# Kernel tuning notes

Hardware: AMD Instinct MI355X
Metric: run time of the kernel (lower is better)

Reference implementation:

```python
import jax, jax.numpy as jnp
import numpy as np

D_MODEL = 1024
NUM_HEADS = 16
D_K = D_MODEL // NUM_HEADS


def setup_inputs() -> dict:
    key = jax.random.key(0)
    ks = jax.random.split(key, 8)
    B, S = 2, 2048
    query = jax.random.normal(ks[0], (B, S, D_MODEL), dtype=jnp.float32)
    k_in = jax.random.normal(ks[1], (B, S, D_MODEL), dtype=jnp.float32)
    value = jax.random.normal(ks[2], (B, S, D_MODEL), dtype=jnp.float32)
    # causal mask: True = masked out (upper triangle above diagonal)
    mask = jnp.triu(jnp.ones((S, S), dtype=bool), k=1)[None, None, :, :]
    scale = 1.0 / np.sqrt(D_MODEL)
    W_q = jax.random.normal(ks[3], (D_MODEL, D_MODEL), dtype=jnp.float32) * scale
    W_k = jax.random.normal(ks[4], (D_MODEL, D_MODEL), dtype=jnp.float32) * scale
    W_v = jax.random.normal(ks[5], (D_MODEL, D_MODEL), dtype=jnp.float32) * scale
    W_o = jax.random.normal(ks[6], (D_MODEL, D_MODEL), dtype=jnp.float32) * scale
    return {"query": query, "key": k_in, "value": value, "mask": mask,
            "W_q": W_q, "W_k": W_k, "W_v": W_v, "W_o": W_o}


def _split(x):
    # [B, S, d_model] -> [B, h, S, d_k]
    B, S, _ = x.shape
    return x.reshape(B, S, NUM_HEADS, D_K).transpose(0, 2, 1, 3)


def reference(query, key, value, mask, W_q, W_k, W_v, W_o):
    # torch nn.Linear(bias=False): y = x @ W.T
    Q = _split(query @ W_q.T)   # [B, h, Sq, d_k]
    K = _split(key @ W_k.T)     # [B, h, Sk, d_k]
    V = _split(value @ W_v.T)   # [B, h, Sk, d_k]
    scores = jnp.einsum('bhqd,bhkd->bhqk', Q, K) / jnp.sqrt(jnp.float32(D_K))
    scores = jnp.where(mask, -jnp.inf, scores)
    attn_w = jax.nn.softmax(scores, axis=-1)
    attn_w = jnp.nan_to_num(attn_w, nan=0.0)
    out = jnp.einsum('bhqk,bhkd->bhqd', attn_w, V)  # [B, h, Sq, d_k]
    B, _, Sq, _ = out.shape
    merged = out.transpose(0, 2, 1, 3).reshape(B, Sq, D_MODEL)
    return merged @ W_o.T
```

## Files before the change

### kernel.cpp

```cpp
#include <hip/hip_runtime.h>
#include <hip/hip_bf16.h>
#include <stdint.h>

typedef __attribute__((ext_vector_type(4))) float f32x4;
typedef __attribute__((ext_vector_type(8))) __bf16 bf16x8;
typedef __attribute__((ext_vector_type(4))) unsigned short us4;
typedef __attribute__((ext_vector_type(8))) unsigned short us8;

#define SEQ 2048
#define DMODEL 1024
#define NH 16
#define DK 64
#define MTOT 4096

__device__ __forceinline__ unsigned short f2bf(float x) {
  union { float f; unsigned int u; } v; v.f = x;
  unsigned int r = v.u + 0x7fffu + ((v.u >> 16) & 1u);
  return (unsigned short)(r >> 16);
}

__device__ __forceinline__ unsigned int cvtpk(float lo, float hi) {
  unsigned int r;
  asm("v_cvt_pk_bf16_f32 %0, %1, %2" : "=v"(r) : "v"(lo), "v"(hi));
  return r;
}

__device__ __forceinline__ f32x4 mfma_bf16(bf16x8 a, bf16x8 b, f32x4 c) {
  return __builtin_amdgcn_mfma_f32_16x16x32_bf16(a, b, c, 0, 0, 0);
}

__device__ __forceinline__ void gload16(const unsigned short* g, unsigned short* l) {
  __builtin_amdgcn_global_load_lds((__attribute__((address_space(1))) void*)g,
                                   (__attribute__((address_space(3))) void*)l,
                                   16, 0, 0);
}

__global__ void cvt_w(const float* __restrict__ s0, const float* __restrict__ s1,
                      const float* __restrict__ s2, const float* __restrict__ s3,
                      unsigned short* __restrict__ d0, unsigned short* __restrict__ d1,
                      unsigned short* __restrict__ d2, unsigned short* __restrict__ d3) {
  const int y = blockIdx.y;
  const float* s = y == 0 ? s0 : y == 1 ? s1 : y == 2 ? s2 : s3;
  unsigned short* d = y == 0 ? d0 : y == 1 ? d1 : y == 2 ? d2 : d3;
  const int n4 = DMODEL * DMODEL / 4;
  const int stride = gridDim.x * blockDim.x;
  for (int i = blockIdx.x * blockDim.x + threadIdx.x; i < n4; i += stride) {
    f32x4 v = reinterpret_cast<const f32x4*>(s)[i];
    us4 o;
    o.x = f2bf(v.x); o.y = f2bf(v.y); o.z = f2bf(v.z); o.w = f2bf(v.w);
    reinterpret_cast<us4*>(d)[i] = o;
  }
}

__global__ __launch_bounds__(256) void gemm_qkv(
    const float* __restrict__ xq, const float* __restrict__ xk, const float* __restrict__ xv,
    const unsigned short* __restrict__ bwq, const unsigned short* __restrict__ bwk,
    const unsigned short* __restrict__ bwv,
    unsigned short* __restrict__ Qh, unsigned short* __restrict__ Kh,
    unsigned short* __restrict__ Vt) {
  const int z = blockIdx.z;
  const float* A = z == 0 ? xq : (z == 1 ? xk : xv);
  const unsigned short* B = z == 0 ? bwq : (z == 1 ? bwk : bwv);
  const float scale = z == 0 ? 0.18033688011112042f : 1.0f;

  __shared__ __align__(16) unsigned short lA[128 * 32];
  __shared__ __align__(16) unsigned short lB[128 * 32];
  const int tid = threadIdx.x;
  const int lane = tid & 63;
  const int wid = tid >> 6;
  const int l15 = lane & 15, l4 = lane >> 4;
  const int bm = blockIdx.x, bn = blockIdx.y;
  const int wr = wid >> 1, wc = wid & 1;

  f32x4 acc[4][4] = {};

  const int chunk0 = (wid * 2 + 0) * 64 + lane;
  const int chunk1 = (wid * 2 + 1) * 64 + lane;
  const int ar0 = chunk0 >> 2, ac0 = chunk0 & 3;
  const int ar1 = chunk1 >> 2, ac1 = chunk1 & 3;
  const float* gAf0 = A + (size_t)(bm * 128 + ar0) * 1024 + ac0 * 8;
  const float* gAf1 = A + (size_t)(bm * 128 + ar1) * 1024 + ac1 * 8;
  const unsigned short* gB0 = B + (size_t)(bn * 128 + ar0) * 1024 + (ac0 ^ (ar0 & 3)) * 8;
  const unsigned short* gB1 = B + (size_t)(bn * 128 + ar1) * 1024 + (ac1 ^ (ar1 & 3)) * 8;
  unsigned short* wA0 = lA + ar0 * 32 + ((ac0 ^ (ar0 & 3)) * 8);
  unsigned short* wA1 = lA + ar1 * 32 + ((ac1 ^ (ar1 & 3)) * 8);
  unsigned short* lB0 = lB + (wid * 2 + 0) * 512;
  unsigned short* lB1 = lB + (wid * 2 + 1) * 512;

  f32x4 ra0 = *reinterpret_cast<const f32x4*>(gAf0);
  f32x4 ra1 = *reinterpret_cast<const f32x4*>(gAf0 + 4);
  f32x4 rb0 = *reinterpret_cast<const f32x4*>(gAf1);
  f32x4 rb1 = *reinterpret_cast<const f32x4*>(gAf1 + 4);

  const int sx = l15 & 3;

  for (int kt = 0; kt < 1024; kt += 32) {
    __syncthreads();
    union { us8 h; unsigned int u[4]; } p0, p1;
    p0.u[0] = cvtpk(ra0.x, ra0.y); p0.u[1] = cvtpk(ra0.z, ra0.w);
    p0.u[2] = cvtpk(ra1.x, ra1.y); p0.u[3] = cvtpk(ra1.z, ra1.w);
    p1.u[0] = cvtpk(rb0.x, rb0.y); p1.u[1] = cvtpk(rb0.z, rb0.w);
    p1.u[2] = cvtpk(rb1.x, rb1.y); p1.u[3] = cvtpk(rb1.z, rb1.w);
    *reinterpret_cast<us8*>(wA0) = p0.h;
    *reinterpret_cast<us8*>(wA1) = p1.h;
    gload16(gB0 + kt, lB0);
    gload16(gB1 + kt, lB1);
    __syncthreads();

    if (kt + 32 < 1024) {
      ra0 = *reinterpret_cast<const f32x4*>(gAf0 + kt + 32);
      ra1 = *reinterpret_cast<const f32x4*>(gAf0 + kt + 36);
      rb0 = *reinterpret_cast<const f32x4*>(gAf1 + kt + 32);
      rb1 = *reinterpret_cast<const f32x4*>(gAf1 + kt + 36);
    }

    bf16x8 af[4], bfr[4];
#pragma unroll
    for (int i = 0; i < 4; ++i)
      af[i] = *reinterpret_cast<const bf16x8*>(
          &lA[(wr * 64 + i * 16 + l15) * 32 + ((l4 ^ sx) * 8)]);
#pragma unroll
    for (int j = 0; j < 4; ++j)
      bfr[j] = *reinterpret_cast<const bf16x8*>(
          &lB[(wc * 64 + j * 16 + l15) * 32 + ((l4 ^ sx) * 8)]);
    if (z < 2) {
#pragma unroll
      for (int i = 0; i < 4; ++i)
#pragma unroll
        for (int j = 0; j < 4; ++j)
          acc[i][j] = mfma_bf16(bfr[j], af[i], acc[i][j]);
    } else {
#pragma unroll
      for (int i = 0; i < 4; ++i)
#pragma unroll
        for (int j = 0; j < 4; ++j)
          acc[i][j] = mfma_bf16(af[i], bfr[j], acc[i][j]);
    }
  }

  const int row0 = bm * 128 + wr * 64;
  const int col0 = bn * 128 + wc * 64;

  if (z < 2) {
    unsigned short* out = z ? Kh : Qh;
#pragma unroll
    for (int i = 0; i < 4; ++i) {
      const int m = row0 + i * 16 + l15;
      const int b = m >> 11, s = m & 2047;
#pragma unroll
      for (int j = 0; j < 4; ++j) {
        const int n0 = col0 + j * 16 + l4 * 4;
        const int h = n0 >> 6, dd = n0 & 63;
        union { us4 h4; unsigned int u[2]; } pk;
        pk.u[0] = cvtpk(acc[i][j][0] * scale, acc[i][j][1] * scale);
        pk.u[1] = cvtpk(acc[i][j][2] * scale, acc[i][j][3] * scale);
        *reinterpret_cast<us4*>(&out[(size_t)(b * NH + h) * (SEQ * DK) + s * DK + dd]) = pk.h4;
      }
    }
  } else {
#pragma unroll
    for (int i = 0; i < 4; ++i) {
      const int m0 = row0 + i * 16 + l4 * 4;
      const int b = m0 >> 11, s0 = m0 & 2047;
      const int g = (s0 >> 2) & 7;
      const int col = (s0 & ~31) + ((g & 3) << 3) + ((g >> 2) << 2);
#pragma unroll
      for (int j = 0; j < 4; ++j) {
        const int n = col0 + j * 16 + l15;
        const int h = n >> 6, dd = n & 63;
        union { us4 h4; unsigned int u[2]; } pk;
        pk.u[0] = cvtpk(acc[i][j][0], acc[i][j][1]);
        pk.u[1] = cvtpk(acc[i][j][2], acc[i][j][3]);
        *reinterpret_cast<us4*>(&Vt[(size_t)(b * NH + h) * (DK * SEQ) + dd * SEQ + col]) = pk.h4;
      }
    }
  }
}

__global__ __launch_bounds__(512) void gemm_o(const unsigned short* __restrict__ A,
                                              const unsigned short* __restrict__ B,
                                              float* __restrict__ out) {
  __shared__ __align__(16) unsigned short lA3[3][128 * 64];
  __shared__ __align__(16) unsigned short lB3[3][128 * 64];

  const int tid = threadIdx.x;
  const int lane = tid & 63, wid = tid >> 6;
  const int l15 = lane & 15, l4 = lane >> 4;
  const int bm = blockIdx.x, bn = blockIdx.y;
  const int wr = wid >> 1, wc = wid & 1;

  f32x4 acc[2][4] = {};

  const int r8 = lane >> 3, c8 = lane & 7;
  const unsigned short* gAs[2];
  const unsigned short* gBs[2];
  int dstoff[2];
#pragma unroll
  for (int is = 0; is < 2; ++is) {
    const int rbase = is * 64 + wid * 8;
    gAs[is] = A + (size_t)(bm * 128 + rbase + r8) * 1024 + (c8 ^ r8) * 8;
    gBs[is] = B + (size_t)(bn * 128 + rbase + r8) * 1024 + (c8 ^ r8) * 8;
    dstoff[is] = rbase * 64;
  }

#define STAGE_O(t, buf)                                         \
  {                                                             \
    const int kb = (t) * 64;                                    \
    gload16(gAs[0] + kb, &lA3[buf][dstoff[0]]);                 \
    gload16(gAs[1] + kb, &lA3[buf][dstoff[1]]);                 \
    gload16(gBs[0] + kb, &lB3[buf][dstoff[0]]);                 \
    gload16(gBs[1] + kb, &lB3[buf][dstoff[1]]);                 \
  }

  STAGE_O(0, 0);
  STAGE_O(1, 1);

#pragma unroll 1
  for (int t = 0; t < 16; ++t) {
    if (t + 1 < 16) {
      asm volatile("s_waitcnt vmcnt(4)" ::: "memory");
    } else {
      asm volatile("s_waitcnt vmcnt(0)" ::: "memory");
    }
    __builtin_amdgcn_sched_barrier(0);
    __builtin_amdgcn_s_barrier();
    __builtin_amdgcn_sched_barrier(0);

    if (t + 2 < 16) {
      const int pb = (t + 2) % 3;
      STAGE_O(t + 2, pb);
    }

    const unsigned short* La = lA3[t % 3];
    const unsigned short* Lb = lB3[t % 3];
#pragma unroll
    for (int kk = 0; kk < 2; ++kk) {
      bf16x8 af[2], bf[4];
#pragma unroll
      for (int i = 0; i < 2; ++i) {
        const int row = wr * 32 + i * 16 + l15;
        af[i] = *reinterpret_cast<const bf16x8*>(
            &La[row * 64 + (((kk * 4 + l4) ^ (l15 & 7)) * 8)]);
      }
#pragma unroll
      for (int j = 0; j < 4; ++j) {
        const int row = wc * 64 + j * 16 + l15;
        bf[j] = *reinterpret_cast<const bf16x8*>(
            &Lb[row * 64 + (((kk * 4 + l4) ^ (l15 & 7)) * 8)]);
      }
#pragma unroll
      for (int i = 0; i < 2; ++i)
#pragma unroll
        for (int j = 0; j < 4; ++j)
          acc[i][j] = mfma_bf16(bf[j], af[i], acc[i][j]);
    }
  }
#undef STAGE_O

  const int row0 = bm * 128 + wr * 32;
  const int col0 = bn * 128 + wc * 64;
#pragma unroll
  for (int i = 0; i < 2; ++i) {
    const int m = row0 + i * 16 + l15;
#pragma unroll
    for (int j = 0; j < 4; ++j) {
      const int n0 = col0 + j * 16 + l4 * 4;
      *reinterpret_cast<f32x4*>(&out[(size_t)m * DMODEL + n0]) = acc[i][j];
    }
  }
}

__global__ __launch_bounds__(512, 2) void attn_kernel(const unsigned short* __restrict__ Qh,
                                                      const unsigned short* __restrict__ Kh,
                                                      const unsigned short* __restrict__ Vt,
                                                      unsigned short* __restrict__ Mg) {
  __shared__ __align__(16) unsigned short Kl[4][64 * 64];
  __shared__ __align__(16) unsigned short Vl[4][64 * 64];

  const int tid = threadIdx.x;
  const int lane = tid & 63;
  const int w = tid >> 6;
  const int l15 = lane & 15, l4 = lane >> 4;

  const int d = blockIdx.x;
  const int xcd = d & 7;
  const int j = d >> 3;
  const int bh = (j >> 3) * 8 + xcd;
  const int x = j & 7;

  const unsigned short* Qb = Qh + (size_t)bh * SEQ * DK;
  const unsigned short* Kb = Kh + (size_t)bh * SEQ * DK;
  const unsigned short* Vb = Vt + (size_t)bh * DK * SEQ;
  const int bq = bh >> 4, hh = bh & 15;
  unsigned short* Mbase = Mg + (size_t)bq * SEQ * DMODEL + hh * DK;

  const int srow = lane >> 3;
  const int sswz = (lane & 7) ^ srow;
  const unsigned short* KsrcB = Kb + (size_t)(w * 8 + srow) * DK + sswz * 8;
  const unsigned short* VsrcB = Vb + (size_t)(w * 8 + srow) * SEQ + sswz * 8;

  const int l7 = l15 & 7;

  const int taus[2] = {15 - x, x};

#pragma unroll 1
  for (int seg = 0; seg < 2; ++seg) {
    const int tau = taus[seg];
    const int qbase = tau * 128;
    const int q0w = qbase + w * 16;
    const int nt = 2 * tau + 2;

    __syncthreads();

    bf16x8 qf0 = *reinterpret_cast<const bf16x8*>(Qb + (size_t)(q0w + l15) * DK + l4 * 8);
    bf16x8 qf1 = *reinterpret_cast<const bf16x8*>(Qb + (size_t)(q0w + l15) * DK + 32 + l4 * 8);

    f32x4 o[4] = {};
    float mrow = -__builtin_inff();
    float lrow = 0.0f;

    gload16(KsrcB, &Kl[0][w * 512]);
    gload16(VsrcB, &Vl[0][w * 512]);
    gload16(KsrcB + (size_t)64 * DK, &Kl[1][w * 512]);
    gload16(VsrcB + 64, &Vl[1][w * 512]);

    const int S = nt >> 1;
#pragma unroll 1
    for (int s = 0; s < S; ++s) {
      const int t0 = s << 1;
      const int kbase0 = t0 << 6;

      asm volatile("s_waitcnt vmcnt(0)" ::: "memory");
      __builtin_amdgcn_sched_barrier(0);
      __builtin_amdgcn_s_barrier();
      __builtin_amdgcn_sched_barrier(0);

      if (t0 + 2 < nt) {
        gload16(KsrcB + (size_t)(kbase0 + 128) * DK, &Kl[(t0 + 2) & 3][w * 512]);
        gload16(VsrcB + (kbase0 + 128), &Vl[(t0 + 2) & 3][w * 512]);
        gload16(KsrcB + (size_t)(kbase0 + 192) * DK, &Kl[(t0 + 3) & 3][w * 512]);
        gload16(VsrcB + (kbase0 + 192), &Vl[(t0 + 3) & 3][w * 512]);
      }

#pragma unroll
      for (int u = 0; u < 2; ++u) {
        const int t = t0 + u;
        const int kbase = t << 6;
        if (kbase >= q0w + 16) continue;
        const unsigned short* Kc = Kl[t & 3];
        const unsigned short* Vc = Vl[t & 3];

        f32x4 sc[4];
        __builtin_amdgcn_s_setprio(1);
#pragma unroll
        for (int c = 0; c < 4; ++c) {
          const int krow = c * 16 + l15;
          bf16x8 kf0 = *reinterpret_cast<const bf16x8*>(&Kc[krow * 64 + ((l4 ^ l7) * 8)]);
          bf16x8 kf1 = *reinterpret_cast<const bf16x8*>(&Kc[krow * 64 + (((4 + l4) ^ l7) * 8)]);
          f32x4 z = {0.f, 0.f, 0.f, 0.f};
          z = mfma_bf16(kf0, qf0, z);
          sc[c] = mfma_bf16(kf1, qf1, z);
        }
        __builtin_amdgcn_s_setprio(0);

        if (kbase + 63 > q0w) {
          const int qg = q0w + l15;
#pragma unroll
          for (int c = 0; c < 4; ++c) {
            const int kp = kbase + c * 16 + l4 * 4;
#pragma unroll
            for (int r = 0; r < 4; ++r)
              if (kp + r > qg) sc[c][r] = -__builtin_inff();
          }
        }

        f32x4 mv = sc[0];
#pragma unroll
        for (int c = 1; c < 4; ++c)
#pragma unroll
          for (int r = 0; r < 4; ++r) mv[r] = fmaxf(mv[r], sc[c][r]);
        float pm = fmaxf(fmaxf(mv[0], mv[1]), fmaxf(mv[2], mv[3]));
        if (!__all(pm - mrow <= 8.0f)) {
          pm = fmaxf(pm, __shfl_xor(pm, 16));
          pm = fmaxf(pm, __shfl_xor(pm, 32));
          const float mn = fmaxf(mrow, pm);
          const float al = __builtin_amdgcn_exp2f(mrow - mn);
          mrow = mn;
          lrow *= al;
#pragma unroll
          for (int dd = 0; dd < 4; ++dd)
#pragma unroll
            for (int r = 0; r < 4; ++r) o[dd][r] *= al;
        }
        union PB { bf16x8 v; unsigned int u[4]; } pbv[2];
        f32x4 sv = {0.f, 0.f, 0.f, 0.f};
#pragma unroll
        for (int c = 0; c < 4; ++c) {
          const float p0 = __builtin_amdgcn_exp2f(sc[c][0] - mrow);
          const float p1 = __builtin_amdgcn_exp2f(sc[c][1] - mrow);
          const float p2 = __builtin_amdgcn_exp2f(sc[c][2] - mrow);
          const float p3 = __builtin_amdgcn_exp2f(sc[c][3] - mrow);
          sv[0] += p0; sv[1] += p1; sv[2] += p2; sv[3] += p3;
          pbv[c >> 1].u[(c & 1) * 2 + 0] = cvtpk(p0, p1);
          pbv[c >> 1].u[(c & 1) * 2 + 1] = cvtpk(p2, p3);
        }
        lrow += (sv[0] + sv[1]) + (sv[2] + sv[3]);

        __builtin_amdgcn_s_setprio(1);
#pragma unroll
        for (int dd = 0; dd < 4; ++dd) {
          const int vrow = dd * 16 + l15;
#pragma unroll
          for (int p = 0; p < 2; ++p) {
            const bf16x8 av = *reinterpret_cast<const bf16x8*>(
                &Vc[vrow * 64 + (((p * 4 + l4) ^ l7) * 8)]);
            o[dd] = mfma_bf16(av, pbv[p].v, o[dd]);
          }
        }
        __builtin_amdgcn_s_setprio(0);
      }
    }

    lrow += __shfl_xor(lrow, 16);
    lrow += __shfl_xor(lrow, 32);
    const float inv = __builtin_amdgcn_rcpf(lrow);
    const int s = q0w + l15;
#pragma unroll
    for (int dd = 0; dd < 4; ++dd) {
      union { us4 h; unsigned int u[2]; } pk;
      pk.u[0] = cvtpk(o[dd][0] * inv, o[dd][1] * inv);
      pk.u[1] = cvtpk(o[dd][2] * inv, o[dd][3] * inv);
      *reinterpret_cast<us4*>(&Mbase[(size_t)s * DMODEL + dd * 16 + l4 * 4]) = pk.h;
    }
  }
}

extern "C" void kernel_launch(void* const* d_in, const int* in_sizes, int n_in,
                              void* d_out, int out_size, void* d_ws, size_t ws_size,
                              hipStream_t stream) {
  (void)in_sizes; (void)n_in; (void)out_size;
  if (ws_size < (size_t)64 * (1 << 20)) return;

  const float* q = (const float*)d_in[0];
  const float* k = (const float*)d_in[1];
  const float* v = (const float*)d_in[2];
  const float* wq = (const float*)d_in[4];
  const float* wk = (const float*)d_in[5];
  const float* wv = (const float*)d_in[6];
  const float* wo = (const float*)d_in[7];

  char* ws = (char*)d_ws;
  unsigned short* bwq = (unsigned short*)(ws + (size_t)24 * (1 << 20));
  unsigned short* bwk = (unsigned short*)(ws + (size_t)26 * (1 << 20));
  unsigned short* bwv = (unsigned short*)(ws + (size_t)28 * (1 << 20));
  unsigned short* bwo = (unsigned short*)(ws + (size_t)30 * (1 << 20));
  unsigned short* Qh  = (unsigned short*)(ws + (size_t)32 * (1 << 20));
  unsigned short* Kh  = (unsigned short*)(ws + (size_t)40 * (1 << 20));
  unsigned short* Vt  = (unsigned short*)(ws + (size_t)48 * (1 << 20));
  unsigned short* Mg  = (unsigned short*)(ws + (size_t)56 * (1 << 20));

  cvt_w<<<dim3(64, 4), 256, 0, stream>>>(wq, wk, wv, wo, bwq, bwk, bwv, bwo);
  gemm_qkv<<<dim3(32, 8, 3), 256, 0, stream>>>(q, k, v, bwq, bwk, bwv, Qh, Kh, Vt);
  attn_kernel<<<dim3(256), 512, 0, stream>>>(Qh, Kh, Vt, Mg);
  gemm_o<<<dim3(32, 8), 512, 0, stream>>>(Mg, bwo, (float*)d_out);
}
```

Before: 126.3 us.

## Pre-convert activations to bf16 and split attention into one q-tile per block

The activation inputs are now converted to bf16 in a separate pass together with the weights, so the QKV GEMM loads both operands with direct global-to-LDS copies instead of loading fp32 through registers and converting inside the main loop. The XOR swizzle on the A/B LDS tiles is dropped, which may bring back LDS bank conflicts. The attention kernel now launches 512 blocks, each handling one query tile, instead of 256 blocks each handling a balanced pair of tiles. This gives more parallelism but loses the per-block pairing that evened out causal work. The extra conversion pass adds a write and re-read of the activations in bf16.

```diff
diff --git a/kernel.cpp b/kernel.cpp
--- a/kernel.cpp
+++ b/kernel.cpp
@@ -5,7 +5,6 @@
 typedef __attribute__((ext_vector_type(4))) float f32x4;
 typedef __attribute__((ext_vector_type(8))) __bf16 bf16x8;
 typedef __attribute__((ext_vector_type(4))) unsigned short us4;
-typedef __attribute__((ext_vector_type(8))) unsigned short us8;
 
 #define SEQ 2048
 #define DMODEL 1024
@@ -35,14 +34,20 @@
                                    16, 0, 0);
 }
 
-__global__ void cvt_w(const float* __restrict__ s0, const float* __restrict__ s1,
-                      const float* __restrict__ s2, const float* __restrict__ s3,
-                      unsigned short* __restrict__ d0, unsigned short* __restrict__ d1,
-                      unsigned short* __restrict__ d2, unsigned short* __restrict__ d3) {
+__global__ void cvt_all(const float* __restrict__ s0, const float* __restrict__ s1,
+                        const float* __restrict__ s2, const float* __restrict__ s3,
+                        const float* __restrict__ s4, const float* __restrict__ s5,
+                        const float* __restrict__ s6,
+                        unsigned short* __restrict__ d0, unsigned short* __restrict__ d1,
+                        unsigned short* __restrict__ d2, unsigned short* __restrict__ d3,
+                        unsigned short* __restrict__ d4, unsigned short* __restrict__ d5,
+                        unsigned short* __restrict__ d6) {
   const int y = blockIdx.y;
-  const float* s = y == 0 ? s0 : y == 1 ? s1 : y == 2 ? s2 : s3;
-  unsigned short* d = y == 0 ? d0 : y == 1 ? d1 : y == 2 ? d2 : d3;
-  const int n4 = DMODEL * DMODEL / 4;
+  const float* s = y == 0 ? s0 : y == 1 ? s1 : y == 2 ? s2 : y == 3 ? s3
+                 : y == 4 ? s4 : y == 5 ? s5 : s6;
+  unsigned short* d = y == 0 ? d0 : y == 1 ? d1 : y == 2 ? d2 : y == 3 ? d3
+                    : y == 4 ? d4 : y == 5 ? d5 : d6;
+  const int n4 = (y < 3) ? (MTOT * DMODEL / 4) : (DMODEL * DMODEL / 4);
   const int stride = gridDim.x * blockDim.x;
   for (int i = blockIdx.x * blockDim.x + threadIdx.x; i < n4; i += stride) {
     f32x4 v = reinterpret_cast<const f32x4*>(s)[i];
@@ -53,13 +58,13 @@
 }
 
 __global__ __launch_bounds__(256) void gemm_qkv(
-    const float* __restrict__ xq, const float* __restrict__ xk, const float* __restrict__ xv,
-    const unsigned short* __restrict__ bwq, const unsigned short* __restrict__ bwk,
-    const unsigned short* __restrict__ bwv,
+    const unsigned short* __restrict__ xq, const unsigned short* __restrict__ xk,
+    const unsigned short* __restrict__ xv, const unsigned short* __restrict__ bwq,
+    const unsigned short* __restrict__ bwk, const unsigned short* __restrict__ bwv,
     unsigned short* __restrict__ Qh, unsigned short* __restrict__ Kh,
     unsigned short* __restrict__ Vt) {
   const int z = blockIdx.z;
-  const float* A = z == 0 ? xq : (z == 1 ? xk : xv);
+  const unsigned short* A = z == 0 ? xq : (z == 1 ? xk : xv);
   const unsigned short* B = z == 0 ? bwq : (z == 1 ? bwk : bwv);
   const float scale = z == 0 ? 0.18033688011112042f : 1.0f;
 
@@ -76,53 +81,29 @@
 
   const int chunk0 = (wid * 2 + 0) * 64 + lane;
   const int chunk1 = (wid * 2 + 1) * 64 + lane;
-  const int ar0 = chunk0 >> 2, ac0 = chunk0 & 3;
-  const int ar1 = chunk1 >> 2, ac1 = chunk1 & 3;
-  const float* gAf0 = A + (size_t)(bm * 128 + ar0) * 1024 + ac0 * 8;
-  const float* gAf1 = A + (size_t)(bm * 128 + ar1) * 1024 + ac1 * 8;
-  const unsigned short* gB0 = B + (size_t)(bn * 128 + ar0) * 1024 + (ac0 ^ (ar0 & 3)) * 8;
-  const unsigned short* gB1 = B + (size_t)(bn * 128 + ar1) * 1024 + (ac1 ^ (ar1 & 3)) * 8;
-  unsigned short* wA0 = lA + ar0 * 32 + ((ac0 ^ (ar0 & 3)) * 8);
-  unsigned short* wA1 = lA + ar1 * 32 + ((ac1 ^ (ar1 & 3)) * 8);
+  const unsigned short* gA0 = A + (size_t)(bm * 128 + (chunk0 >> 2)) * 1024 + (chunk0 & 3) * 8;
+  const unsigned short* gA1 = A + (size_t)(bm * 128 + (chunk1 >> 2)) * 1024 + (chunk1 & 3) * 8;
+  const unsigned short* gB0 = B + (size_t)(bn * 128 + (chunk0 >> 2)) * 1024 + (chunk0 & 3) * 8;
+  const unsigned short* gB1 = B + (size_t)(bn * 128 + (chunk1 >> 2)) * 1024 + (chunk1 & 3) * 8;
+  unsigned short* lA0 = lA + (wid * 2 + 0) * 512;
+  unsigned short* lA1 = lA + (wid * 2 + 1) * 512;
   unsigned short* lB0 = lB + (wid * 2 + 0) * 512;
   unsigned short* lB1 = lB + (wid * 2 + 1) * 512;
 
-  f32x4 ra0 = *reinterpret_cast<const f32x4*>(gAf0);
-  f32x4 ra1 = *reinterpret_cast<const f32x4*>(gAf0 + 4);
-  f32x4 rb0 = *reinterpret_cast<const f32x4*>(gAf1);
-  f32x4 rb1 = *reinterpret_cast<const f32x4*>(gAf1 + 4);
-
-  const int sx = l15 & 3;
-
   for (int kt = 0; kt < 1024; kt += 32) {
     __syncthreads();
-    union { us8 h; unsigned int u[4]; } p0, p1;
-    p0.u[0] = cvtpk(ra0.x, ra0.y); p0.u[1] = cvtpk(ra0.z, ra0.w);
-    p0.u[2] = cvtpk(ra1.x, ra1.y); p0.u[3] = cvtpk(ra1.z, ra1.w);
-    p1.u[0] = cvtpk(rb0.x, rb0.y); p1.u[1] = cvtpk(rb0.z, rb0.w);
-    p1.u[2] = cvtpk(rb1.x, rb1.y); p1.u[3] = cvtpk(rb1.z, rb1.w);
-    *reinterpret_cast<us8*>(wA0) = p0.h;
-    *reinterpret_cast<us8*>(wA1) = p1.h;
+    gload16(gA0 + kt, lA0);
+    gload16(gA1 + kt, lA1);
     gload16(gB0 + kt, lB0);
     gload16(gB1 + kt, lB1);
     __syncthreads();
-
-    if (kt + 32 < 1024) {
-      ra0 = *reinterpret_cast<const f32x4*>(gAf0 + kt + 32);
-      ra1 = *reinterpret_cast<const f32x4*>(gAf0 + kt + 36);
-      rb0 = *reinterpret_cast<const f32x4*>(gAf1 + kt + 32);
-      rb1 = *reinterpret_cast<const f32x4*>(gAf1 + kt + 36);
-    }
-
     bf16x8 af[4], bfr[4];
 #pragma unroll
     for (int i = 0; i < 4; ++i)
-      af[i] = *reinterpret_cast<const bf16x8*>(
-          &lA[(wr * 64 + i * 16 + l15) * 32 + ((l4 ^ sx) * 8)]);
+      af[i] = *reinterpret_cast<const bf16x8*>(&lA[(wr * 64 + i * 16 + l15) * 32 + l4 * 8]);
 #pragma unroll
     for (int j = 0; j < 4; ++j)
-      bfr[j] = *reinterpret_cast<const bf16x8*>(
-          &lB[(wc * 64 + j * 16 + l15) * 32 + ((l4 ^ sx) * 8)]);
+      bfr[j] = *reinterpret_cast<const bf16x8*>(&lB[(wc * 64 + j * 16 + l15) * 32 + l4 * 8]);
     if (z < 2) {
 #pragma unroll
       for (int i = 0; i < 4; ++i)
@@ -283,10 +264,13 @@
   const int l15 = lane & 15, l4 = lane >> 4;
 
   const int d = blockIdx.x;
-  const int xcd = d & 7;
-  const int j = d >> 3;
-  const int bh = (j >> 3) * 8 + xcd;
-  const int x = j & 7;
+  const int base = d & 255;
+  const int pair = d >> 8;
+  const int xcd = base & 7;
+  const int jj = base >> 3;
+  const int bh = (jj >> 3) * 8 + xcd;
+  const int qi = jj & 7;
+  const int tau = pair ? qi : 15 - qi;
 
   const unsigned short* Qb = Qh + (size_t)bh * SEQ * DK;
   const unsigned short* Kb = Kh + (size_t)bh * SEQ * DK;
@@ -301,137 +285,129 @@
 
   const int l7 = l15 & 7;
 
-  const int taus[2] = {15 - x, x};
-
+  const int qbase = tau * 128;
+  const int q0w = qbase + w * 16;
+  const int nt = 2 * tau + 2;
+
+  bf16x8 qf0 = *reinterpret_cast<const bf16x8*>(Qb + (size_t)(q0w + l15) * DK + l4 * 8);
+  bf16x8 qf1 = *reinterpret_cast<const bf16x8*>(Qb + (size_t)(q0w + l15) * DK + 32 + l4 * 8);
+
+  f32x4 o[4] = {};
+  float mrow = -__builtin_inff();
+  float lrow = 0.0f;
+
+  gload16(KsrcB, &Kl[0][w * 512]);
+  gload16(VsrcB, &Vl[0][w * 512]);
+  gload16(KsrcB + (size_t)64 * DK, &Kl[1][w * 512]);
+  gload16(VsrcB + 64, &Vl[1][w * 512]);
+
+  const int S = nt >> 1;
 #pragma unroll 1
-  for (int seg = 0; seg < 2; ++seg) {
-    const int tau = taus[seg];
-    const int qbase = tau * 128;
-    const int q0w = qbase + w * 16;
-    const int nt = 2 * tau + 2;
-
-    __syncthreads();
-
-    bf16x8 qf0 = *reinterpret_cast<const bf16x8*>(Qb + (size_t)(q0w + l15) * DK + l4 * 8);
-    bf16x8 qf1 = *reinterpret_cast<const bf16x8*>(Qb + (size_t)(q0w + l15) * DK + 32 + l4 * 8);
-
-    f32x4 o[4] = {};
-    float mrow = -__builtin_inff();
-    float lrow = 0.0f;
-
-    gload16(KsrcB, &Kl[0][w * 512]);
-    gload16(VsrcB, &Vl[0][w * 512]);
-    gload16(KsrcB + (size_t)64 * DK, &Kl[1][w * 512]);
-    gload16(VsrcB + 64, &Vl[1][w * 512]);
-
-    const int S = nt >> 1;
-#pragma unroll 1
-    for (int s = 0; s < S; ++s) {
-      const int t0 = s << 1;
-      const int kbase0 = t0 << 6;
-
-      asm volatile("s_waitcnt vmcnt(0)" ::: "memory");
-      __builtin_amdgcn_sched_barrier(0);
-      __builtin_amdgcn_s_barrier();
-      __builtin_amdgcn_sched_barrier(0);
-
-      if (t0 + 2 < nt) {
-        gload16(KsrcB + (size_t)(kbase0 + 128) * DK, &Kl[(t0 + 2) & 3][w * 512]);
-        gload16(VsrcB + (kbase0 + 128), &Vl[(t0 + 2) & 3][w * 512]);
-        gload16(KsrcB + (size_t)(kbase0 + 192) * DK, &Kl[(t0 + 3) & 3][w * 512]);
-        gload16(VsrcB + (kbase0 + 192), &Vl[(t0 + 3) & 3][w * 512]);
-      }
-
-#pragma unroll
-      for (int u = 0; u < 2; ++u) {
-        const int t = t0 + u;
-        const int kbase = t << 6;
-        if (kbase >= q0w + 16) continue;
-        const unsigned short* Kc = Kl[t & 3];
-        const unsigned short* Vc = Vl[t & 3];
-
-        f32x4 sc[4];
-        __builtin_amdgcn_s_setprio(1);
+  for (int s = 0; s < S; ++s) {
+    const int t0 = s << 1;
+    const int kbase0 = t0 << 6;
+
+    asm volatile("s_waitcnt vmcnt(0)" ::: "memory");
+    __builtin_amdgcn_sched_barrier(0);
+    __builtin_amdgcn_s_barrier();
+    __builtin_amdgcn_sched_barrier(0);
+
+    if (t0 + 2 < nt) {
+      gload16(KsrcB + (size_t)(kbase0 + 128) * DK, &Kl[(t0 + 2) & 3][w * 512]);
+      gload16(VsrcB + (kbase0 + 128), &Vl[(t0 + 2) & 3][w * 512]);
+      gload16(KsrcB + (size_t)(kbase0 + 192) * DK, &Kl[(t0 + 3) & 3][w * 512]);
+      gload16(VsrcB + (kbase0 + 192), &Vl[(t0 + 3) & 3][w * 512]);
+    }
+
+#pragma unroll
+    for (int u = 0; u < 2; ++u) {
+      const int t = t0 + u;
+      const int kbase = t << 6;
+      if (kbase >= q0w + 16) continue;
+      const unsigned short* Kc = Kl[t & 3];
+      const unsigned short* Vc = Vl[t & 3];
+
+      f32x4 sc[4];
+      __builtin_amdgcn_s_setprio(1);
+#pragma unroll
+      for (int c = 0; c < 4; ++c) {
+        const int krow = c * 16 + l15;
+        bf16x8 kf0 = *reinterpret_cast<const bf16x8*>(&Kc[krow * 64 + ((l4 ^ l7) * 8)]);
+        bf16x8 kf1 = *reinterpret_cast<const bf16x8*>(&Kc[krow * 64 + (((4 + l4) ^ l7) * 8)]);
+        f32x4 z = {0.f, 0.f, 0.f, 0.f};
+        z = mfma_bf16(kf0, qf0, z);
+        sc[c] = mfma_bf16(kf1, qf1, z);
+      }
+      __builtin_amdgcn_s_setprio(0);
+
+      if (kbase + 63 > q0w) {
+        const int qg = q0w + l15;
 #pragma unroll
         for (int c = 0; c < 4; ++c) {
-          const int krow = c * 16 + l15;
-          bf16x8 kf0 = *reinterpret_cast<const bf16x8*>(&Kc[krow * 64 + ((l4 ^ l7) * 8)]);
-          bf16x8 kf1 = *reinterpret_cast<const bf16x8*>(&Kc[krow * 64 + (((4 + l4) ^ l7) * 8)]);
-          f32x4 z = {0.f, 0.f, 0.f, 0.f};
-          z = mfma_bf16(kf0, qf0, z);
-          sc[c] = mfma_bf16(kf1, qf1, z);
+          const int kp = kbase + c * 16 + l4 * 4;
+#pragma unroll
+          for (int r = 0; r < 4; ++r)
+            if (kp + r > qg) sc[c][r] = -__builtin_inff();
         }
-        __builtin_amdgcn_s_setprio(0);
-
-        if (kbase + 63 > q0w) {
-          const int qg = q0w + l15;
-#pragma unroll
-          for (int c = 0; c < 4; ++c) {
-            const int kp = kbase + c * 16 + l4 * 4;
-#pragma unroll
-            for (int r = 0; r < 4; ++r)
-              if (kp + r > qg) sc[c][r] = -__builtin_inff();
-          }
+      }
+
+      f32x4 mv = sc[0];
+#pragma unroll
+      for (int c = 1; c < 4; ++c)
+#pragma unroll
+        for (int r = 0; r < 4; ++r) mv[r] = fmaxf(mv[r], sc[c][r]);
+      float pm = fmaxf(fmaxf(mv[0], mv[1]), fmaxf(mv[2], mv[3]));
+      if (!__all(pm - mrow <= 8.0f)) {
+        pm = fmaxf(pm, __shfl_xor(pm, 16));
+        pm = fmaxf(pm, __shfl_xor(pm, 32));
+        const float mn = fmaxf(mrow, pm);
+        const float al = __builtin_amdgcn_exp2f(mrow - mn);
+        mrow = mn;
+        lrow *= al;
+#pragma unroll
+        for (int dd = 0; dd < 4; ++dd)
+#pragma unroll
+          for (int r = 0; r < 4; ++r) o[dd][r] *= al;
+      }
+      union PB { bf16x8 v; unsigned int u[4]; } pbv[2];
+      f32x4 sv = {0.f, 0.f, 0.f, 0.f};
+#pragma unroll
+      for (int c = 0; c < 4; ++c) {
+        const float p0 = __builtin_amdgcn_exp2f(sc[c][0] - mrow);
+        const float p1 = __builtin_amdgcn_exp2f(sc[c][1] - mrow);
+        const float p2 = __builtin_amdgcn_exp2f(sc[c][2] - mrow);
+        const float p3 = __builtin_amdgcn_exp2f(sc[c][3] - mrow);
+        sv[0] += p0; sv[1] += p1; sv[2] += p2; sv[3] += p3;
+        pbv[c >> 1].u[(c & 1) * 2 + 0] = cvtpk(p0, p1);
+        pbv[c >> 1].u[(c & 1) * 2 + 1] = cvtpk(p2, p3);
+      }
+      lrow += (sv[0] + sv[1]) + (sv[2] + sv[3]);
+
+      __builtin_amdgcn_s_setprio(1);
+#pragma unroll
+      for (int dd = 0; dd < 4; ++dd) {
+        const int vrow = dd * 16 + l15;
+#pragma unroll
+        for (int p = 0; p < 2; ++p) {
+          const bf16x8 av = *reinterpret_cast<const bf16x8*>(
+              &Vc[vrow * 64 + (((p * 4 + l4) ^ l7) * 8)]);
+          o[dd] = mfma_bf16(av, pbv[p].v, o[dd]);
         }
-
-        f32x4 mv = sc[0];
-#pragma unroll
-        for (int c = 1; c < 4; ++c)
-#pragma unroll
-          for (int r = 0; r < 4; ++r) mv[r] = fmaxf(mv[r], sc[c][r]);
-        float pm = fmaxf(fmaxf(mv[0], mv[1]), fmaxf(mv[2], mv[3]));
-        if (!__all(pm - mrow <= 8.0f)) {
-          pm = fmaxf(pm, __shfl_xor(pm, 16));
-          pm = fmaxf(pm, __shfl_xor(pm, 32));
-          const float mn = fmaxf(mrow, pm);
-          const float al = __builtin_amdgcn_exp2f(mrow - mn);
-          mrow = mn;
-          lrow *= al;
-#pragma unroll
-          for (int dd = 0; dd < 4; ++dd)
-#pragma unroll
-            for (int r = 0; r < 4; ++r) o[dd][r] *= al;
-        }
-        union PB { bf16x8 v; unsigned int u[4]; } pbv[2];
-        f32x4 sv = {0.f, 0.f, 0.f, 0.f};
-#pragma unroll
-        for (int c = 0; c < 4; ++c) {
-          const float p0 = __builtin_amdgcn_exp2f(sc[c][0] - mrow);
-          const float p1 = __builtin_amdgcn_exp2f(sc[c][1] - mrow);
-          const float p2 = __builtin_amdgcn_exp2f(sc[c][2] - mrow);
-          const float p3 = __builtin_amdgcn_exp2f(sc[c][3] - mrow);
-          sv[0] += p0; sv[1] += p1; sv[2] += p2; sv[3] += p3;
-          pbv[c >> 1].u[(c & 1) * 2 + 0] = cvtpk(p0, p1);
-          pbv[c >> 1].u[(c & 1) * 2 + 1] = cvtpk(p2, p3);
-        }
-        lrow += (sv[0] + sv[1]) + (sv[2] + sv[3]);
-
-        __builtin_amdgcn_s_setprio(1);
-#pragma unroll
-        for (int dd = 0; dd < 4; ++dd) {
-          const int vrow = dd * 16 + l15;
-#pragma unroll
-          for (int p = 0; p < 2; ++p) {
-            const bf16x8 av = *reinterpret_cast<const bf16x8*>(
-                &Vc[vrow * 64 + (((p * 4 + l4) ^ l7) * 8)]);
-            o[dd] = mfma_bf16(av, pbv[p].v, o[dd]);
-          }
-        }
-        __builtin_amdgcn_s_setprio(0);
-      }
-    }
-
-    lrow += __shfl_xor(lrow, 16);
-    lrow += __shfl_xor(lrow, 32);
-    const float inv = __builtin_amdgcn_rcpf(lrow);
-    const int s = q0w + l15;
-#pragma unroll
-    for (int dd = 0; dd < 4; ++dd) {
-      union { us4 h; unsigned int u[2]; } pk;
-      pk.u[0] = cvtpk(o[dd][0] * inv, o[dd][1] * inv);
-      pk.u[1] = cvtpk(o[dd][2] * inv, o[dd][3] * inv);
-      *reinterpret_cast<us4*>(&Mbase[(size_t)s * DMODEL + dd * 16 + l4 * 4]) = pk.h;
-    }
+      }
+      __builtin_amdgcn_s_setprio(0);
+    }
+  }
+
+  lrow += __shfl_xor(lrow, 16);
+  lrow += __shfl_xor(lrow, 32);
+  const float inv = __builtin_amdgcn_rcpf(lrow);
+  const int s = q0w + l15;
+#pragma unroll
+  for (int dd = 0; dd < 4; ++dd) {
+    union { us4 h; unsigned int u[2]; } pk;
+    pk.u[0] = cvtpk(o[dd][0] * inv, o[dd][1] * inv);
+    pk.u[1] = cvtpk(o[dd][2] * inv, o[dd][3] * inv);
+    *reinterpret_cast<us4*>(&Mbase[(size_t)s * DMODEL + dd * 16 + l4 * 4]) = pk.h;
   }
 }
 
@@ -450,6 +426,9 @@
   const float* wo = (const float*)d_in[7];
 
   char* ws = (char*)d_ws;
+  unsigned short* xq  = (unsigned short*)(ws + (size_t)0  * (1 << 20));
+  unsigned short* xk  = (unsigned short*)(ws + (size_t)8  * (1 << 20));
+  unsigned short* xv  = (unsigned short*)(ws + (size_t)16 * (1 << 20));
   unsigned short* bwq = (unsigned short*)(ws + (size_t)24 * (1 << 20));
   unsigned short* bwk = (unsigned short*)(ws + (size_t)26 * (1 << 20));
   unsigned short* bwv = (unsigned short*)(ws + (size_t)28 * (1 << 20));
@@ -459,8 +438,9 @@
   unsigned short* Vt  = (unsigned short*)(ws + (size_t)48 * (1 << 20));
   unsigned short* Mg  = (unsigned short*)(ws + (size_t)56 * (1 << 20));
 
-  cvt_w<<<dim3(64, 4), 256, 0, stream>>>(wq, wk, wv, wo, bwq, bwk, bwv, bwo);
-  gemm_qkv<<<dim3(32, 8, 3), 256, 0, stream>>>(q, k, v, bwq, bwk, bwv, Qh, Kh, Vt);
-  attn_kernel<<<dim3(256), 512, 0, stream>>>(Qh, Kh, Vt, Mg);
+  cvt_all<<<dim3(512, 7), 256, 0, stream>>>(q, k, v, wq, wk, wv, wo,
+                                            xq, xk, xv, bwq, bwk, bwv, bwo);
+  gemm_qkv<<<dim3(32, 8, 3), 256, 0, stream>>>(xq, xk, xv, bwq, bwk, bwv, Qh, Kh, Vt);
+  attn_kernel<<<dim3(512), 512, 0, stream>>>(Qh, Kh, Vt, Mg);
   gemm_o<<<dim3(32, 8), 512, 0, stream>>>(Mg, bwo, (float*)d_out);
 }
```

Measured after the change: 119.8 us. -5.1%, faster.
